# Performance work log

Measured on AMD Instinct MI355X. Metric: run time of the kernel, lower is better.

Reference implementation:

```python
import jax, jax.numpy as jnp
import numpy as np

# Stochastic-computing layer: values in [0,1] are encoded as random bitstreams
# (bit = uniform <= value), multiply = AND, and the reduction over input rows is
# a chained random MUX (tf.where with p=0.5 coins), then mean over the bit axis.
BATCH, D_IN, D_OUT, BIT_SIZE = 512, 1024, 1024, 128


def setup_inputs() -> dict:
    key = jax.random.key(0)
    kx, kw = jax.random.split(key)
    # bitstream-encoded probabilities in [0, 1]
    x = jax.random.uniform(kx, (BATCH, D_IN), dtype=jnp.float32)
    w = jax.random.uniform(kw, (D_IN, D_OUT), dtype=jnp.float32)
    return {"x": x, "w": w}


def reference(x, w):
    B, Din = x.shape
    Dout = w.shape[1]
    key = jax.random.key(42)
    kx, kw, kc = jax.random.split(key, 3)

    # bitstream generation: bit = (uniform <= value)
    x_bits = jax.random.uniform(kx, (B, Din, BIT_SIZE)) <= x[:, :, None]        # (B, Din, T) bool
    w_bits = jax.random.uniform(kw, (Din, Dout, BIT_SIZE)) <= w[:, :, None]     # (Din, Dout, T) bool

    # Chained random MUX over rows 1..Din-2 (mirrors `for row in range(1, dim-1)`):
    #   final = where(coin, final, row_r)  ->  result is row r of the LAST step
    #   whose coin was False; row 0 if every coin was True. Coins are shared
    #   across the output dim (original select_line shape (B, 1, T)).
    n_steps = Din - 2
    coins = jax.random.uniform(kc, (n_steps, B, BIT_SIZE)) <= 0.5               # (steps, B, T) bool
    rows = jnp.arange(1, Din - 1)                                               # (steps,)
    idx = jnp.max(jnp.where(~coins, rows[:, None, None], 0), axis=0)            # (B, T) int

    # Gather the selected row's bits instead of materializing (B, Din, Dout, T)
    chosen_x = jnp.take_along_axis(x_bits, idx[:, None, :], axis=1)[:, 0, :]    # (B, T)
    w_bt = jnp.transpose(w_bits, (0, 2, 1))                                     # (Din, T, Dout)
    chosen_w = w_bt[idx, jnp.arange(BIT_SIZE)[None, :], :]                      # (B, T, Dout)

    # stochastic multiply (AND) then decode via mean over the bit axis
    final = (chosen_x[:, :, None] & chosen_w).astype(jnp.float32)               # (B, T, Dout)
    return jnp.mean(final, axis=1)                                              # (B, Dout)
```

## Files before the change

### kernel.cpp

```cpp
#include <hip/hip_runtime.h>
#include <stdint.h>

#define BATCH 512
#define D_IN 1024
#define D_OUT 1024
#define BITSZ 128
#define N_STEPS (D_IN - 2)

#define IBASE 960
#define ICAP 64

#define WS_V_OFF 0u
#define WS_V_BYTES (BATCH * BITSZ * 4u)
#define WS_TAB_OFF (WS_V_OFF + WS_V_BYTES)
#define WS_TAB_BYTES (BITSZ * ICAP * 32u * 4u)
#define WS_NEEDED (WS_TAB_OFF + WS_TAB_BYTES)

__host__ __device__ __forceinline__ uint32_t rotl32(uint32_t x, uint32_t d) {
  return (x << d) | (x >> (32u - d));
}

__host__ __device__ __forceinline__ void threefry2x32(uint32_t k0, uint32_t k1,
                                                      uint32_t& x0, uint32_t& x1) {
  const uint32_t k2 = k0 ^ k1 ^ 0x1BD11BDAu;
  x0 += k0; x1 += k1;
#define TFR(r) { x0 += x1; x1 = rotl32(x1, (r)); x1 ^= x0; }
  TFR(13) TFR(15) TFR(26) TFR(6)
  x0 += k1; x1 += k2 + 1u;
  TFR(17) TFR(29) TFR(16) TFR(24)
  x0 += k2; x1 += k0 + 2u;
  TFR(13) TFR(15) TFR(26) TFR(6)
  x0 += k0; x1 += k1 + 3u;
  TFR(17) TFR(29) TFR(16) TFR(24)
  x0 += k1; x1 += k2 + 4u;
  TFR(13) TFR(15) TFR(26) TFR(6)
  x0 += k2; x1 += k0 + 5u;
#undef TFR
}

__device__ __forceinline__ float runif(uint32_t k0, uint32_t k1, uint32_t n) {
  uint32_t x0 = 0u, x1 = n;
  threefry2x32(k0, k1, x0, x1);
  const uint32_t b = x0 ^ x1;
  return __uint_as_float((b >> 9) | 0x3f800000u) - 1.0f;
}

__global__ void __launch_bounds__(1024) k_front(const float* __restrict__ x,
                                                int* __restrict__ v,
                                                uint32_t* __restrict__ tab,
                                                uint32_t ck0, uint32_t ck1,
                                                uint32_t xk0, uint32_t xk1,
                                                uint32_t wk0, uint32_t wk1,
                                                const float* __restrict__ w,
                                                int use_tab) {
  const int t = blockIdx.x;
  const int tid = threadIdx.x;

  __shared__ uint32_t s_bm[2];
  if (tid < 2) s_bm[tid] = 0u;
  __syncthreads();

  if (tid < BATCH) {
    const int b = tid;
    int idx = 0;
    for (int s = N_STEPS - 1; s >= 0; --s) {
      const float u = runif(ck0, ck1,
          ((uint32_t)s << 16) + ((uint32_t)b << 7) + (uint32_t)t);
      if (u > 0.5f) { idx = s + 1; break; }
    }
    const float ux = runif(xk0, xk1,
        ((uint32_t)b << 17) + ((uint32_t)idx << 7) + (uint32_t)t);
    const int xb = (ux <= x[b * D_IN + idx]) ? 1 : 0;
    v[b * BITSZ + t] = xb ? idx : -1;
    if (xb && idx >= IBASE) {
      const int bp = idx - IBASE;
      atomicOr(&s_bm[bp >> 5], 1u << (bp & 31));
    }
  }
  __syncthreads();

  if (!use_tab) return;

  unsigned long long bm = (unsigned long long)s_bm[0] |
                          ((unsigned long long)s_bm[1] << 32);
  const int d = tid;
  const int lane = tid & 63;
  const int wv = tid >> 6;
  while (bm) {
    const int j = __builtin_ctzll(bm);
    bm &= bm - 1ull;
    const int i = IBASE + j;
    const float u = runif(wk0, wk1,
        ((uint32_t)i << 17) + ((uint32_t)d << 7) + (uint32_t)t);
    const unsigned long long mb = __ballot(u <= w[i * D_OUT + d]);
    uint32_t* row = tab + (((t << 6) + j) << 5);
    if (lane == 0)  row[wv * 2]     = (uint32_t)mb;
    if (lane == 32) row[wv * 2 + 1] = (uint32_t)(mb >> 32);
  }
}

__global__ void __launch_bounds__(1024) k_acc(const float* __restrict__ w,
                                              const int* __restrict__ v,
                                              const uint32_t* __restrict__ tab,
                                              float* __restrict__ out,
                                              uint32_t wk0, uint32_t wk1,
                                              int use_tab) {
  const int b = blockIdx.x;
  const int tid = threadIdx.x;

  __shared__ uint32_t s_tab[BITSZ * 32];
  __shared__ int s_list[BITSZ];
  __shared__ int s_wcnt[2];
  __shared__ int s_anyfb;

  if (tid == 0) s_anyfb = 0;
  __syncthreads();

  unsigned long long mb = 0;
  int code = -1;
  bool act = false;
  if (tid < BITSZ) {
    code = v[b * BITSZ + tid];
    act = code >= 0;
    mb = __ballot(act);
    if ((tid & 63) == 0) s_wcnt[tid >> 6] = __popcll(mb);
  }
  __syncthreads();
  const int m = s_wcnt[0] + s_wcnt[1];
  if (tid < BITSZ && act) {
    const int lane = tid & 63;
    const int pos = ((tid >= 64) ? s_wcnt[0] : 0) +
                    __popcll(mb & ((1ull << lane) - 1ull));
    s_list[pos] = (code << 7) | tid;
    if (!(use_tab && code >= IBASE)) atomicOr(&s_anyfb, 1);
  }
  __syncthreads();

  const int wrd = tid & 31;
  for (int jj = tid >> 5; jj < m; jj += 32) {
    const int e = s_list[jj];
    const int i = e >> 7, t = e & 127;
    if (use_tab && i >= IBASE)
      s_tab[(jj << 5) + wrd] = tab[(((t << 6) + (i - IBASE)) << 5) + wrd];
  }
  __syncthreads();

  const int dw = tid >> 5, db = tid & 31;
  int acc = 0;
  if (s_anyfb == 0) {
#pragma unroll 4
    for (int jj = 0; jj < m; ++jj)
      acc += (s_tab[(jj << 5) + dw] >> db) & 1u;
  } else {
    for (int jj = 0; jj < m; ++jj) {
      const int e = s_list[jj];
      const int i = e >> 7, t = e & 127;
      if (use_tab && i >= IBASE) {
        acc += (s_tab[(jj << 5) + dw] >> db) & 1u;
      } else {
        const float u = runif(wk0, wk1,
            ((uint32_t)i << 17) + ((uint32_t)tid << 7) + (uint32_t)t);
        acc += (u <= w[i * D_OUT + tid]) ? 1 : 0;
      }
    }
  }
  out[b * D_OUT + tid] = (float)acc * (1.0f / (float)BITSZ);
}

struct TFKeys { uint32_t xk0, xk1, wk0, wk1, ck0, ck1; };

static TFKeys derive_keys() {
  TFKeys K;
  uint32_t a0 = 0, a1 = 0; threefry2x32(0u, 42u, a0, a1); K.xk0 = a0; K.xk1 = a1;
  uint32_t b0 = 0, b1 = 1; threefry2x32(0u, 42u, b0, b1); K.wk0 = b0; K.wk1 = b1;
  uint32_t c0 = 0, c1 = 2; threefry2x32(0u, 42u, c0, c1); K.ck0 = c0; K.ck1 = c1;
  return K;
}

extern "C" void kernel_launch(void* const* d_in, const int* in_sizes, int n_in,
                              void* d_out, int out_size, void* d_ws, size_t ws_size,
                              hipStream_t stream) {
  const float* x = (const float*)d_in[0];
  const float* w = (const float*)d_in[1];
  if (n_in >= 2 && in_sizes[0] == D_IN * D_OUT && in_sizes[1] == BATCH * D_IN) {
    const float* tmp = x; x = w; w = tmp;
  }
  float* out = (float*)d_out;
  char* ws = (char*)d_ws;
  int* v = (int*)(ws + WS_V_OFF);
  uint32_t* tab = (uint32_t*)(ws + WS_TAB_OFF);

  const int use_tab = (ws_size >= WS_NEEDED) ? 1 : 0;
  const TFKeys K = derive_keys();

  hipLaunchKernelGGL(k_front, dim3(BITSZ), dim3(1024), 0, stream,
                     x, v, tab, K.ck0, K.ck1, K.xk0, K.xk1, K.wk0, K.wk1,
                     w, use_tab);
  hipLaunchKernelGGL(k_acc, dim3(BATCH), dim3(D_OUT), 0, stream,
                     w, v, tab, out, K.wk0, K.wk1, use_tab);
}
```

Measured before the change: 24.81 us.

## Split front kernel into index and table kernels, transpose LDS table for vector reads

The single front kernel becomes two. k_idx uses 256 blocks of 256 threads, one thread per (batch, bit) pair, and unrolls the coin search four steps at a time. k_tab builds the weight-bit table over 512 blocks, recomputing the row bitmap from v with wave-level OR reductions. In k_acc the shared table is stored column-major with a padded stride so each thread reads four entries with one uint4 load. This spreads work over more CUs than the old 128-block launch, but adds a third kernel launch and a pass that rereads v.

```diff
diff --git a/kernel.cpp b/kernel.cpp
--- a/kernel.cpp
+++ b/kernel.cpp
@@ -15,6 +15,9 @@
 #define WS_TAB_OFF (WS_V_OFF + WS_V_BYTES)
 #define WS_TAB_BYTES (BITSZ * ICAP * 32u * 4u)
 #define WS_NEEDED (WS_TAB_OFF + WS_TAB_BYTES)
+
+#define MCAP 128
+#define TSTRIDE 132
 
 __host__ __device__ __forceinline__ uint32_t rotl32(uint32_t x, uint32_t d) {
   return (x << d) | (x >> (32u - d));
@@ -45,47 +48,70 @@
   return __uint_as_float((b >> 9) | 0x3f800000u) - 1.0f;
 }
 
-__global__ void __launch_bounds__(1024) k_front(const float* __restrict__ x,
-                                                int* __restrict__ v,
-                                                uint32_t* __restrict__ tab,
-                                                uint32_t ck0, uint32_t ck1,
-                                                uint32_t xk0, uint32_t xk1,
-                                                uint32_t wk0, uint32_t wk1,
-                                                const float* __restrict__ w,
-                                                int use_tab) {
-  const int t = blockIdx.x;
+__global__ void __launch_bounds__(256) k_idx(const float* __restrict__ x,
+                                             int* __restrict__ v,
+                                             uint32_t ck0, uint32_t ck1,
+                                             uint32_t xk0, uint32_t xk1) {
+  const int tid = blockIdx.x * 256 + threadIdx.x;
+  const int b = tid >> 7;
+  const int t = tid & 127;
+
+  int idx = 0;
+  int s;
+  for (s = N_STEPS - 1; s >= 3; s -= 4) {
+    const float u0 = runif(ck0, ck1, ((uint32_t)(s)     << 16) + (uint32_t)tid);
+    const float u1 = runif(ck0, ck1, ((uint32_t)(s - 1) << 16) + (uint32_t)tid);
+    const float u2 = runif(ck0, ck1, ((uint32_t)(s - 2) << 16) + (uint32_t)tid);
+    const float u3 = runif(ck0, ck1, ((uint32_t)(s - 3) << 16) + (uint32_t)tid);
+    if (u0 > 0.5f) { idx = s + 1; break; }
+    if (u1 > 0.5f) { idx = s;     break; }
+    if (u2 > 0.5f) { idx = s - 1; break; }
+    if (u3 > 0.5f) { idx = s - 2; break; }
+  }
+  if (idx == 0 && s < 3) {
+    const float u0 = runif(ck0, ck1, (1u << 16) + (uint32_t)tid);
+    const float u1 = runif(ck0, ck1, (uint32_t)tid);
+    if (u0 > 0.5f)      idx = 2;
+    else if (u1 > 0.5f) idx = 1;
+  }
+
+  const float ux = runif(xk0, xk1,
+      ((uint32_t)b << 17) + ((uint32_t)idx << 7) + (uint32_t)t);
+  const int xb = (ux <= x[b * D_IN + idx]) ? 1 : 0;
+  v[tid] = xb ? idx : -1;
+}
+
+__global__ void __launch_bounds__(256) k_tab(const float* __restrict__ w,
+                                             const int* __restrict__ v,
+                                             uint32_t* __restrict__ tab,
+                                             uint32_t wk0, uint32_t wk1) {
+  const int t = blockIdx.x >> 2;
+  const int q = blockIdx.x & 3;
   const int tid = threadIdx.x;
 
   __shared__ uint32_t s_bm[2];
   if (tid < 2) s_bm[tid] = 0u;
   __syncthreads();
 
-  if (tid < BATCH) {
-    const int b = tid;
-    int idx = 0;
-    for (int s = N_STEPS - 1; s >= 0; --s) {
-      const float u = runif(ck0, ck1,
-          ((uint32_t)s << 16) + ((uint32_t)b << 7) + (uint32_t)t);
-      if (u > 0.5f) { idx = s + 1; break; }
-    }
-    const float ux = runif(xk0, xk1,
-        ((uint32_t)b << 17) + ((uint32_t)idx << 7) + (uint32_t)t);
-    const int xb = (ux <= x[b * D_IN + idx]) ? 1 : 0;
-    v[b * BITSZ + t] = xb ? idx : -1;
-    if (xb && idx >= IBASE) {
-      const int bp = idx - IBASE;
-      atomicOr(&s_bm[bp >> 5], 1u << (bp & 31));
-    }
-  }
-  __syncthreads();
-
-  if (!use_tab) return;
+  unsigned long long m64 = 0;
+  {
+    const int v0 = v[tid * BITSZ + t];
+    const int v1 = v[(tid + 256) * BITSZ + t];
+    if (v0 >= IBASE) m64 |= 1ull << (v0 - IBASE);
+    if (v1 >= IBASE) m64 |= 1ull << (v1 - IBASE);
+  }
+  for (int off = 32; off; off >>= 1) m64 |= __shfl_down(m64, off);
+  if ((tid & 63) == 0) {
+    atomicOr(&s_bm[0], (uint32_t)m64);
+    atomicOr(&s_bm[1], (uint32_t)(m64 >> 32));
+  }
+  __syncthreads();
 
   unsigned long long bm = (unsigned long long)s_bm[0] |
                           ((unsigned long long)s_bm[1] << 32);
-  const int d = tid;
+  const int d = q * 256 + tid;
   const int lane = tid & 63;
-  const int wv = tid >> 6;
+  const int wbase = (d >> 5) & ~1;
   while (bm) {
     const int j = __builtin_ctzll(bm);
     bm &= bm - 1ull;
@@ -94,8 +120,8 @@
         ((uint32_t)i << 17) + ((uint32_t)d << 7) + (uint32_t)t);
     const unsigned long long mb = __ballot(u <= w[i * D_OUT + d]);
     uint32_t* row = tab + (((t << 6) + j) << 5);
-    if (lane == 0)  row[wv * 2]     = (uint32_t)mb;
-    if (lane == 32) row[wv * 2 + 1] = (uint32_t)(mb >> 32);
+    if (lane == 0)  row[wbase]     = (uint32_t)mb;
+    if (lane == 32) row[wbase + 1] = (uint32_t)(mb >> 32);
   }
 }
 
@@ -108,12 +134,12 @@
   const int b = blockIdx.x;
   const int tid = threadIdx.x;
 
-  __shared__ uint32_t s_tab[BITSZ * 32];
+  __shared__ __align__(16) uint32_t s_tab2[32 * TSTRIDE];
   __shared__ int s_list[BITSZ];
   __shared__ int s_wcnt[2];
   __shared__ int s_anyfb;
 
-  if (tid == 0) s_anyfb = 0;
+  if (tid == 0) s_anyfb = use_tab ? 0 : 1;
   __syncthreads();
 
   unsigned long long mb = 0;
@@ -127,44 +153,49 @@
   }
   __syncthreads();
   const int m = s_wcnt[0] + s_wcnt[1];
+  const int m4 = (m + 3) & ~3;
   if (tid < BITSZ && act) {
     const int lane = tid & 63;
     const int pos = ((tid >= 64) ? s_wcnt[0] : 0) +
                     __popcll(mb & ((1ull << lane) - 1ull));
     s_list[pos] = (code << 7) | tid;
-    if (!(use_tab && code >= IBASE)) atomicOr(&s_anyfb, 1);
-  }
-  __syncthreads();
-
-  const int wrd = tid & 31;
-  for (int jj = tid >> 5; jj < m; jj += 32) {
-    const int e = s_list[jj];
-    const int i = e >> 7, t = e & 127;
-    if (use_tab && i >= IBASE)
-      s_tab[(jj << 5) + wrd] = tab[(((t << 6) + (i - IBASE)) << 5) + wrd];
-  }
-  __syncthreads();
-
-  const int dw = tid >> 5, db = tid & 31;
-  int acc = 0;
+    if (code < IBASE) atomicOr(&s_anyfb, 1);
+  }
+  __syncthreads();
+
   if (s_anyfb == 0) {
-#pragma unroll 4
-    for (int jj = 0; jj < m; ++jj)
-      acc += (s_tab[(jj << 5) + dw] >> db) & 1u;
+    const int wrd = tid & 31;
+    for (int jj = tid >> 5; jj < m; jj += 32) {
+      const int e = s_list[jj];
+      const int i = e >> 7, t = e & 127;
+      s_tab2[wrd * TSTRIDE + jj] = tab[(((t << 6) + (i - IBASE)) << 5) + wrd];
+    }
+    if (tid < 32)
+      for (int jj = m; jj < m4; ++jj) s_tab2[tid * TSTRIDE + jj] = 0u;
+    __syncthreads();
+
+    const int dw = tid >> 5, db = tid & 31;
+    const uint32_t* colp = &s_tab2[dw * TSTRIDE];
+    int acc = 0;
+    for (int k = 0; k < m4; k += 4) {
+      const uint4 r = *(const uint4*)(colp + k);
+      acc += (r.x >> db) & 1u;
+      acc += (r.y >> db) & 1u;
+      acc += (r.z >> db) & 1u;
+      acc += (r.w >> db) & 1u;
+    }
+    out[b * D_OUT + tid] = (float)acc * (1.0f / (float)BITSZ);
   } else {
+    int acc = 0;
     for (int jj = 0; jj < m; ++jj) {
       const int e = s_list[jj];
       const int i = e >> 7, t = e & 127;
-      if (use_tab && i >= IBASE) {
-        acc += (s_tab[(jj << 5) + dw] >> db) & 1u;
-      } else {
-        const float u = runif(wk0, wk1,
-            ((uint32_t)i << 17) + ((uint32_t)tid << 7) + (uint32_t)t);
-        acc += (u <= w[i * D_OUT + tid]) ? 1 : 0;
-      }
+      const float u = runif(wk0, wk1,
+          ((uint32_t)i << 17) + ((uint32_t)tid << 7) + (uint32_t)t);
+      acc += (u <= w[i * D_OUT + tid]) ? 1 : 0;
     }
-  }
-  out[b * D_OUT + tid] = (float)acc * (1.0f / (float)BITSZ);
+    out[b * D_OUT + tid] = (float)acc * (1.0f / (float)BITSZ);
+  }
 }
 
 struct TFKeys { uint32_t xk0, xk1, wk0, wk1, ck0, ck1; };
@@ -193,9 +224,11 @@
   const int use_tab = (ws_size >= WS_NEEDED) ? 1 : 0;
   const TFKeys K = derive_keys();
 
-  hipLaunchKernelGGL(k_front, dim3(BITSZ), dim3(1024), 0, stream,
-                     x, v, tab, K.ck0, K.ck1, K.xk0, K.xk1, K.wk0, K.wk1,
-                     w, use_tab);
+  hipLaunchKernelGGL(k_idx, dim3((BATCH * BITSZ) / 256), dim3(256), 0, stream,
+                     x, v, K.ck0, K.ck1, K.xk0, K.xk1);
+  if (use_tab)
+    hipLaunchKernelGGL(k_tab, dim3(BITSZ * 4), dim3(256), 0, stream,
+                       w, v, tab, K.wk0, K.wk1);
   hipLaunchKernelGGL(k_acc, dim3(BATCH), dim3(D_OUT), 0, stream,
                      w, v, tab, out, K.wk0, K.wk1, use_tab);
 }
```

Result: faster. 22.47 us (-9.4%).
